# Kernel tuning notes

Measured on AMD Instinct MI355X. Metric: run time of the kernel, lower is better.

The kernel has to match this reference:

```python
import jax, jax.numpy as jnp
import numpy as np

D, E, H, K = 1024, 8, 4096, 2
B, S = 4, 2048


def setup_inputs() -> dict:
    key = jax.random.key(0)
    ks = jax.random.split(key, 5)
    scale = 0.02
    return {
        "x": jax.random.normal(ks[0], (B, S, D), dtype=jnp.float32),
        "gate_w": jax.random.normal(ks[1], (D, E), dtype=jnp.float32) * scale,
        "w1": jax.random.normal(ks[2], (E, D, H), dtype=jnp.float32) * scale,
        "b1": jnp.zeros((E, H), dtype=jnp.float32),
        "w2": jax.random.normal(ks[3], (E, H, D), dtype=jnp.float32) * scale,
        "b2": jnp.zeros((E, D), dtype=jnp.float32),
        "top_k": K,
    }


def reference(x, gate_w, w1, b1, w2, b2, top_k):
    orig_shape = x.shape
    d = x.shape[-1]
    xt = x.reshape(-1, d)                      # [T, D]
    T = xt.shape[0]

    # Gating: top-k over expert scores, softmax over the selected k.
    scores = xt @ gate_w                       # [T, E]
    expert_weights, expert_indices = jax.lax.top_k(scores, top_k)  # [T, K]
    expert_weights = jax.nn.softmax(expert_weights, axis=-1)

    # Dense all-expert MLP (GPT-style fc -> GELU -> proj), batched over experts.
    h = jnp.einsum('td,edh->eth', xt, w1) + b1[:, None, :]   # [E, T, H]
    h = jax.nn.gelu(h, approximate=False)
    outs = jnp.einsum('eth,ehd->etd', h, w2) + b2[:, None, :]  # [E, T, D]

    # Combine: gather each token's selected experts and mix with gate weights.
    tok = jnp.arange(T)[:, None]               # [T, 1]
    gathered = outs[expert_indices, tok]       # [T, K, D]
    y = jnp.sum(gathered * expert_weights[..., None], axis=1)  # [T, D]
    return y.reshape(orig_shape)
```

## Files before the change

### kernel.cpp

```cpp
#include <hip/hip_runtime.h>
#include <stdint.h>

#define T_TOK 8192
#define D_DIM 1024
#define E_NUM 8
#define H_DIM 4096

#define BM 128
#define BN 128
#define BK 64
#define NSEG 8
#define MAX_ROWS2 17408
#define MAX_MT2 (MAX_ROWS2/BM)
#define KSPLIT 2

typedef unsigned short u16;
typedef __attribute__((ext_vector_type(8))) short shortx8;
typedef __attribute__((ext_vector_type(4))) float floatx4;
typedef __attribute__((ext_vector_type(8))) unsigned short ushortx8;

typedef const __attribute__((address_space(1))) unsigned int g_uint;
typedef __attribute__((address_space(3))) unsigned int l_uint;

__device__ __forceinline__ u16 f2bf(float f) {
  union { float f; unsigned int u; } v; v.f = f;
  unsigned int r = v.u + 0x7FFFu + ((v.u >> 16) & 1u);
  return (u16)(r >> 16);
}
__device__ __forceinline__ void gld_lds16(const u16* g, u16* l) {
  __builtin_amdgcn_global_load_lds((g_uint*)g, (l_uint*)l, 16, 0, 0);
}
__device__ __forceinline__ float gelu_fast(float v) {
  float y = v * (1.5957691216f + 0.07135481627f * v * v);
  y = fminf(y, 30.f);
  float ey = __expf(y);
  return v * ey * __builtin_amdgcn_rcpf(1.f + ey);
}

__global__ __launch_bounds__(256) void init_kernel(int* counts, int* fills, int* row_token) {
  int i = blockIdx.x * 256 + threadIdx.x;
  if (i < MAX_ROWS2) row_token[i] = -1;
  if (blockIdx.x == 0 && threadIdx.x < NSEG) { counts[threadIdx.x] = 0; fills[threadIdx.x] = 0; }
}

__global__ __launch_bounds__(256) void zero4_kernel(float4* out) {
  out[(size_t)blockIdx.x * 256 + threadIdx.x] = float4{0.f, 0.f, 0.f, 0.f};
}

__global__ __launch_bounds__(256) void convert_x_kernel(const float* __restrict__ X, u16* __restrict__ XC) {
  size_t i = ((size_t)blockIdx.x * 256 + threadIdx.x) * 8;
  float4 a = *(const float4*)&X[i];
  float4 b = *(const float4*)&X[i + 4];
  ushortx8 o;
  o[0] = f2bf(a.x); o[1] = f2bf(a.y); o[2] = f2bf(a.z); o[3] = f2bf(a.w);
  o[4] = f2bf(b.x); o[5] = f2bf(b.y); o[6] = f2bf(b.z); o[7] = f2bf(b.w);
  *(ushortx8*)&XC[i] = o;
}

__global__ __launch_bounds__(256) void gate_kernel(const float* __restrict__ X, const float* __restrict__ GW,
                                                   int* __restrict__ tk_idx, float* __restrict__ tk_w,
                                                   int* __restrict__ counts) {
  const int lane = threadIdx.x & 63;
  const int t = blockIdx.x * 4 + (threadIdx.x >> 6);
  const float4* xr4 = (const float4*)(X + (size_t)t * D_DIM + lane * 16);
  const float4* gw4 = (const float4*)GW;
  float acc[E_NUM];
#pragma unroll
  for (int e = 0; e < E_NUM; e++) acc[e] = 0.f;
#pragma unroll
  for (int i4 = 0; i4 < 4; i4++) {
    float4 xv = xr4[i4];
#pragma unroll
    for (int c = 0; c < 4; c++) {
      float xs = (&xv.x)[c];
      int d = lane * 16 + i4 * 4 + c;
      float4 g0 = gw4[d * 2], g1 = gw4[d * 2 + 1];
      acc[0] += xs * g0.x; acc[1] += xs * g0.y; acc[2] += xs * g0.z; acc[3] += xs * g0.w;
      acc[4] += xs * g1.x; acc[5] += xs * g1.y; acc[6] += xs * g1.z; acc[7] += xs * g1.w;
    }
  }
#pragma unroll
  for (int e = 0; e < E_NUM; e++)
    for (int off = 32; off; off >>= 1) acc[e] += __shfl_xor(acc[e], off);
  if (lane == 0) {
    int i0 = 0; float v0 = acc[0];
#pragma unroll
    for (int e = 1; e < E_NUM; e++) if (acc[e] > v0) { v0 = acc[e]; i0 = e; }
    int i1 = -1; float v1 = -1e30f;
#pragma unroll
    for (int e = 0; e < E_NUM; e++) if (e != i0 && acc[e] > v1) { v1 = acc[e]; i1 = e; }
    float e1 = expf(v1 - v0);
    float inv = 1.f / (1.f + e1);
    tk_idx[t * 2] = i0; tk_idx[t * 2 + 1] = i1;
    tk_w[t * 2] = inv;  tk_w[t * 2 + 1] = e1 * inv;
    atomicAdd(&counts[i0], 1); atomicAdd(&counts[i1], 1);
  }
}

__global__ void prefix_kernel(const int* counts, int* seg) {
  if (threadIdx.x == 0 && blockIdx.x == 0) {
    int a = 0;
    for (int i = 0; i < NSEG; i++) { seg[i] = a; a += ((counts[i] + BM - 1) / BM) * BM; }
    seg[NSEG] = a;
  }
}

__global__ __launch_bounds__(256) void fill_kernel(const int* __restrict__ tk_idx, const float* __restrict__ tk_w,
                                                   const int* __restrict__ seg, int* __restrict__ fills,
                                                   int* __restrict__ row_token, float* __restrict__ row_weight) {
  int t = blockIdx.x * 256 + threadIdx.x;
  if (t >= T_TOK) return;
#pragma unroll
  for (int s = 0; s < 2; s++) {
    int sidx = tk_idx[t * 2 + s];
    int pos = atomicAdd(&fills[sidx], 1);
    int r = seg[sidx] + pos;
    row_token[r] = t; row_weight[r] = tk_w[t * 2 + s];
  }
}

__global__ __launch_bounds__(256) void transpose_kernel(const float* __restrict__ src, u16* __restrict__ dst,
                                                        int R, int C) {
  __shared__ u16 tile[32][33];
  int tx = threadIdx.x & 31, ty = threadIdx.x >> 5;
  size_t off = (size_t)blockIdx.z * R * C;
  int r0 = blockIdx.y * 32, c0 = blockIdx.x * 32;
#pragma unroll
  for (int i = 0; i < 32; i += 8) tile[ty + i][tx] = f2bf(src[off + (size_t)(r0 + ty + i) * C + c0 + tx]);
  __syncthreads();
#pragma unroll
  for (int i = 0; i < 32; i += 8) dst[off + (size_t)(c0 + ty + i) * R + r0 + tx] = tile[tx][ty + i];
}

__global__ __launch_bounds__(256, 3) void fc1_kernel(const u16* __restrict__ XC, const u16* __restrict__ W1T,
                                                     const float* __restrict__ B1, u16* __restrict__ Hbuf,
                                                     const int* __restrict__ row_token, const int* __restrict__ seg,
                                                     int mtile0, int e_filter) {
  const int mtile = mtile0 + blockIdx.y, ntile = blockIdx.x;
  const int row0 = mtile * BM;
  if (row0 >= seg[NSEG]) return;
  int sidx = 0;
#pragma unroll
  for (int i = 1; i < NSEG; i++) if (row0 >= seg[i]) sidx = i;
  const int e = sidx;
  if (e_filter >= 0 && e != e_filter) return;
  const size_t ebase = (e_filter >= 0) ? 0 : (size_t)e * H_DIM;
  const u16* Bbase = W1T + (ebase + (size_t)ntile * BN) * D_DIM;

  __shared__ u16 lA[BM * BK];
  __shared__ u16 lB[BN * BK];
  const int tid = threadIdx.x;
  const u16* gA[4]; const u16* gB[4];
#pragma unroll
  for (int r = 0; r < 4; r++) {
    int c = r * 256 + tid;
    int arow = c >> 3, acol = (c & 7) * 8;
    int tok = row_token[row0 + arow]; if (tok < 0) tok = 0;
    gA[r] = XC + (size_t)tok * D_DIM + acol;
    gB[r] = Bbase + (size_t)arow * D_DIM + acol;
  }
  const int lane = tid & 63;
  const int mq = (tid >> 7) & 1, nq = (tid >> 6) & 1;
  const int lrow = lane & 15, quad = lane >> 4;
  floatx4 acc[4][4];
#pragma unroll
  for (int i = 0; i < 4; i++)
#pragma unroll
    for (int j = 0; j < 4; j++)
#pragma unroll
      for (int r = 0; r < 4; r++) acc[i][j][r] = 0.f;

  for (int k0 = 0; k0 < D_DIM; k0 += BK) {
#pragma unroll
    for (int r = 0; r < 4; r++) gld_lds16(gA[r] + k0, &lA[(r * 256 + tid) * 8]);
#pragma unroll
    for (int r = 0; r < 4; r++) gld_lds16(gB[r] + k0, &lB[(r * 256 + tid) * 8]);
    __syncthreads();
#pragma unroll
    for (int kk = 0; kk < 2; kk++) {
      shortx8 af[4], bfr[4];
#pragma unroll
      for (int i = 0; i < 4; i++) af[i]  = *(const shortx8*)&lA[(mq * 64 + i * 16 + lrow) * BK + kk * 32 + quad * 8];
#pragma unroll
      for (int i = 0; i < 4; i++) bfr[i] = *(const shortx8*)&lB[(nq * 64 + i * 16 + lrow) * BK + kk * 32 + quad * 8];
#pragma unroll
      for (int i = 0; i < 4; i++)
#pragma unroll
        for (int j = 0; j < 4; j++)
          acc[i][j] = __builtin_amdgcn_mfma_f32_16x16x32_bf16(af[i], bfr[j], acc[i][j], 0, 0, 0);
    }
    __syncthreads();
  }
#pragma unroll
  for (int j = 0; j < 4; j++) {
    float bv = B1[(size_t)e * H_DIM + ntile * BN + nq * 64 + j * 16 + lrow];
#pragma unroll
    for (int i = 0; i < 4; i++)
#pragma unroll
      for (int rr = 0; rr < 4; rr++) {
        int hrow = (mtile - mtile0) * BM + mq * 64 + i * 16 + quad * 4 + rr;
        float v = acc[i][j][rr] + bv;
        Hbuf[(size_t)hrow * H_DIM + (size_t)ntile * BN + nq * 64 + j * 16 + lrow] = f2bf(gelu_fast(v));
      }
  }
}

__global__ __launch_bounds__(256, 3) void fc2_kernel(const u16* __restrict__ Hbuf, const u16* __restrict__ W2T,
                                                     const float* __restrict__ B2, float* __restrict__ out,
                                                     const int* __restrict__ row_token, const float* __restrict__ row_weight,
                                                     const int* __restrict__ seg,
                                                     int mtile0, int e_filter) {
  const int mtile = mtile0 + blockIdx.y, ntile = blockIdx.x;
  const int kz = blockIdx.z;
  const int row0 = mtile * BM;
  if (row0 >= seg[NSEG]) return;
  int sidx = 0;
#pragma unroll
  for (int i = 1; i < NSEG; i++) if (row0 >= seg[i]) sidx = i;
  const int e = sidx;
  if (e_filter >= 0 && e != e_filter) return;
  const size_t ebase = (e_filter >= 0) ? 0 : (size_t)e * D_DIM;
  const u16* Bbase = W2T + (ebase + (size_t)ntile * BN) * H_DIM;

  __shared__ u16 lA[BM * BK];
  __shared__ u16 lB[BN * BK];
  const int tid = threadIdx.x;
  const u16* gA[4]; const u16* gB[4];
#pragma unroll
  for (int r = 0; r < 4; r++) {
    int c = r * 256 + tid;
    int arow = c >> 3, acol = (c & 7) * 8;
    gA[r] = Hbuf + (size_t)((mtile - mtile0) * BM + arow) * H_DIM + acol;
    gB[r] = Bbase + (size_t)arow * H_DIM + acol;
  }
  const int lane = tid & 63;
  const int mq = (tid >> 7) & 1, nq = (tid >> 6) & 1;
  const int lrow = lane & 15, quad = lane >> 4;
  floatx4 acc[4][4];
#pragma unroll
  for (int i = 0; i < 4; i++)
#pragma unroll
    for (int j = 0; j < 4; j++)
#pragma unroll
      for (int r = 0; r < 4; r++) acc[i][j][r] = 0.f;

  const int kbeg = kz * (H_DIM / KSPLIT);
  const int kend = kbeg + (H_DIM / KSPLIT);
  for (int k0 = kbeg; k0 < kend; k0 += BK) {
#pragma unroll
    for (int r = 0; r < 4; r++) gld_lds16(gA[r] + k0, &lA[(r * 256 + tid) * 8]);
#pragma unroll
    for (int r = 0; r < 4; r++) gld_lds16(gB[r] + k0, &lB[(r * 256 + tid) * 8]);
    __syncthreads();
#pragma unroll
    for (int kk = 0; kk < 2; kk++) {
      shortx8 af[4], bfr[4];
#pragma unroll
      for (int i = 0; i < 4; i++) af[i]  = *(const shortx8*)&lA[(mq * 64 + i * 16 + lrow) * BK + kk * 32 + quad * 8];
#pragma unroll
      for (int i = 0; i < 4; i++) bfr[i] = *(const shortx8*)&lB[(nq * 64 + i * 16 + lrow) * BK + kk * 32 + quad * 8];
#pragma unroll
      for (int i = 0; i < 4; i++)
#pragma unroll
        for (int j = 0; j < 4; j++)
          acc[i][j] = __builtin_amdgcn_mfma_f32_16x16x32_bf16(af[i], bfr[j], acc[i][j], 0, 0, 0);
    }
    __syncthreads();
  }
#pragma unroll
  for (int i = 0; i < 4; i++)
#pragma unroll
    for (int rr = 0; rr < 4; rr++) {
      int gr = row0 + mq * 64 + i * 16 + quad * 4 + rr;
      int tok = row_token[gr];
      if (tok >= 0) {
        float wgt = row_weight[gr];
        size_t base = (size_t)tok * D_DIM + (size_t)ntile * BN + nq * 64 + lrow;
#pragma unroll
        for (int j = 0; j < 4; j++) {
          float bv = (kz == 0) ? B2[(size_t)e * D_DIM + ntile * BN + nq * 64 + j * 16 + lrow] : 0.f;
          float val = (acc[i][j][rr] + bv) * wgt;
          unsafeAtomicAdd(&out[base + j * 16], val);
        }
      }
    }
}

extern "C" void kernel_launch(void* const* d_in, const int* in_sizes, int n_in,
                              void* d_out, int out_size, void* d_ws, size_t ws_size,
                              hipStream_t stream) {
  const float* x  = (const float*)d_in[0];
  const float* gw = (const float*)d_in[1];
  const float* w1 = (const float*)d_in[2];
  const float* b1 = (const float*)d_in[3];
  const float* w2 = (const float*)d_in[4];
  const float* b2 = (const float*)d_in[5];
  float* out = (float*)d_out;

  char* p = (char*)d_ws;
  auto alloc = [&](size_t n) { char* q = p; p += (n + 255) & ~(size_t)255; return q; };
  int*   counts     = (int*)alloc(NSEG * 4);
  int*   fills      = (int*)alloc(NSEG * 4);
  int*   seg        = (int*)alloc((NSEG + 1) * 4);
  int*   tk_idx     = (int*)alloc((size_t)T_TOK * 2 * 4);
  float* tk_w       = (float*)alloc((size_t)T_TOK * 2 * 4);
  int*   row_token  = (int*)alloc((size_t)MAX_ROWS2 * 4);
  float* row_weight = (float*)alloc((size_t)MAX_ROWS2 * 4);
  u16*   xc         = (u16*)alloc((size_t)T_TOK * D_DIM * 2);
  size_t meta = (size_t)(p - (char*)d_ws);

  const size_t Wfull = (size_t)E_NUM * H_DIM * D_DIM * 2;
  const size_t Wone  = (size_t)H_DIM * D_DIM * 2;
  auto hbytes = [](int n) { int cmx = (MAX_MT2 + n - 1) / n; return (size_t)cmx * BM * H_DIM * 2; };

  int mode = 3, N = 1;
  {
    const int cand[6] = {1, 2, 4, 8, 16, 32};
    for (int ci = 0; ci < 6 && mode == 3; ci++)
      if (meta + 2 * Wfull + hbytes(cand[ci]) <= ws_size) { mode = 0; N = cand[ci]; }
    for (int ci = 0; ci < 6 && mode == 3; ci++)
      if (meta + Wfull + hbytes(cand[ci]) <= ws_size) { mode = 1; N = cand[ci]; }
    for (int ci = 0; ci < 6 && mode == 3; ci++)
      if (meta + Wone + hbytes(cand[ci]) <= ws_size) { mode = 2; N = cand[ci]; }
  }

  if (mode == 3) {
    zero4_kernel<<<(int)(((size_t)T_TOK * D_DIM) / 1024), 256, 0, stream>>>((float4*)out);
    return;
  }

  u16 *W1T, *W2T;
  if (mode == 0) { W1T = (u16*)alloc(Wfull); W2T = (u16*)alloc(Wfull); }
  else           { W1T = W2T = (u16*)alloc(mode == 1 ? Wfull : Wone); }
  u16* Hbuf = (u16*)alloc(hbytes(N));
  const int cm = (MAX_MT2 + N - 1) / N;

  init_kernel<<<(MAX_ROWS2 + 255) / 256, 256, 0, stream>>>(counts, fills, row_token);
  convert_x_kernel<<<(int)(((size_t)T_TOK * D_DIM) / 2048), 256, 0, stream>>>(x, xc);
  gate_kernel<<<T_TOK / 4, 256, 0, stream>>>(x, gw, tk_idx, tk_w, counts);
  prefix_kernel<<<1, 64, 0, stream>>>(counts, seg);
  fill_kernel<<<T_TOK / 256, 256, 0, stream>>>(tk_idx, tk_w, seg, fills, row_token, row_weight);
  zero4_kernel<<<(int)(((size_t)T_TOK * D_DIM) / 1024), 256, 0, stream>>>((float4*)out);

  if (mode == 0) {
    transpose_kernel<<<dim3(H_DIM / 32, D_DIM / 32, E_NUM), 256, 0, stream>>>(w1, W1T, D_DIM, H_DIM);
    transpose_kernel<<<dim3(D_DIM / 32, H_DIM / 32, E_NUM), 256, 0, stream>>>(w2, W2T, H_DIM, D_DIM);
  }

  for (int c = 0; c < N; ++c) {
    int mtile0 = c * cm;
    int cmc = MAX_MT2 - mtile0; if (cmc > cm) cmc = cm; if (cmc <= 0) break;
    if (mode == 0) {
      fc1_kernel<<<dim3(H_DIM / BN, cmc), 256, 0, stream>>>(xc, W1T, b1, Hbuf, row_token, seg, mtile0, -1);
      fc2_kernel<<<dim3(D_DIM / BN, cmc, KSPLIT), 256, 0, stream>>>(Hbuf, W2T, b2, out, row_token, row_weight, seg, mtile0, -1);
    } else if (mode == 1) {
      transpose_kernel<<<dim3(H_DIM / 32, D_DIM / 32, E_NUM), 256, 0, stream>>>(w1, W1T, D_DIM, H_DIM);
      fc1_kernel<<<dim3(H_DIM / BN, cmc), 256, 0, stream>>>(xc, W1T, b1, Hbuf, row_token, seg, mtile0, -1);
      transpose_kernel<<<dim3(D_DIM / 32, H_DIM / 32, E_NUM), 256, 0, stream>>>(w2, W2T, H_DIM, D_DIM);
      fc2_kernel<<<dim3(D_DIM / BN, cmc, KSPLIT), 256, 0, stream>>>(Hbuf, W2T, b2, out, row_token, row_weight, seg, mtile0, -1);
    } else {
      for (int e = 0; e < E_NUM; e++) {
        transpose_kernel<<<dim3(H_DIM / 32, D_DIM / 32, 1), 256, 0, stream>>>(w1 + (size_t)e * D_DIM * H_DIM, W1T, D_DIM, H_DIM);
        fc1_kernel<<<dim3(H_DIM / BN, cmc), 256, 0, stream>>>(xc, W1T, b1, Hbuf, row_token, seg, mtile0, e);
      }
      for (int e = 0; e < E_NUM; e++) {
        transpose_kernel<<<dim3(D_DIM / 32, H_DIM / 32, 1), 256, 0, stream>>>(w2 + (size_t)e * H_DIM * D_DIM, W2T, H_DIM, D_DIM);
        fc2_kernel<<<dim3(D_DIM / BN, cmc, KSPLIT), 256, 0, stream>>>(Hbuf, W2T, b2, out, row_token, row_weight, seg, mtile0, e);
      }
    }
  }
}
```

Measured before the change: 1.085 ms.

## Replace split-K atomic scatter with per-row output buffer and combine kernel

fc2 no longer splits K or atomically adds into the output. Each routed row now writes its weighted result to a row-indexed buffer, and a new combine kernel sums each token's two expert rows using a row_of map recorded in fill_kernel. This drops the output zeroing and the float atomics, at the cost of an extra buffer write/read and half as many fc2 blocks. The weight transpose kernel also moves to 64x64 tiles with float4 loads and 8-wide bf16 stores. The larger workspace allocation could push mode selection toward a less favourable mode.

```diff
diff --git a/kernel.cpp b/kernel.cpp
--- a/kernel.cpp
+++ b/kernel.cpp
@@ -12,7 +12,6 @@
 #define NSEG 8
 #define MAX_ROWS2 17408
 #define MAX_MT2 (MAX_ROWS2/BM)
-#define KSPLIT 2
 
 typedef unsigned short u16;
 typedef __attribute__((ext_vector_type(8))) short shortx8;
@@ -107,7 +106,8 @@
 
 __global__ __launch_bounds__(256) void fill_kernel(const int* __restrict__ tk_idx, const float* __restrict__ tk_w,
                                                    const int* __restrict__ seg, int* __restrict__ fills,
-                                                   int* __restrict__ row_token, float* __restrict__ row_weight) {
+                                                   int* __restrict__ row_token, float* __restrict__ row_weight,
+                                                   int* __restrict__ row_of) {
   int t = blockIdx.x * 256 + threadIdx.x;
   if (t >= T_TOK) return;
 #pragma unroll
@@ -116,20 +116,34 @@
     int pos = atomicAdd(&fills[sidx], 1);
     int r = seg[sidx] + pos;
     row_token[r] = t; row_weight[r] = tk_w[t * 2 + s];
+    row_of[t * 2 + s] = r;
   }
 }
 
 __global__ __launch_bounds__(256) void transpose_kernel(const float* __restrict__ src, u16* __restrict__ dst,
                                                         int R, int C) {
-  __shared__ u16 tile[32][33];
-  int tx = threadIdx.x & 31, ty = threadIdx.x >> 5;
-  size_t off = (size_t)blockIdx.z * R * C;
-  int r0 = blockIdx.y * 32, c0 = blockIdx.x * 32;
-#pragma unroll
-  for (int i = 0; i < 32; i += 8) tile[ty + i][tx] = f2bf(src[off + (size_t)(r0 + ty + i) * C + c0 + tx]);
+  __shared__ u16 tile[64][68];
+  const int tid = threadIdx.x;
+  size_t off = (size_t)blockIdx.z * (size_t)R * C;
+  int r0 = blockIdx.y * 64, c0 = blockIdx.x * 64;
+  int rr = tid >> 4, cc = (tid & 15) * 4;
+#pragma unroll
+  for (int i = 0; i < 4; i++) {
+    int r = rr + i * 16;
+    float4 v = *(const float4*)&src[off + (size_t)(r0 + r) * C + c0 + cc];
+    u16* tp = &tile[r][cc];
+    tp[0] = f2bf(v.x); tp[1] = f2bf(v.y); tp[2] = f2bf(v.z); tp[3] = f2bf(v.w);
+  }
   __syncthreads();
-#pragma unroll
-  for (int i = 0; i < 32; i += 8) dst[off + (size_t)(c0 + ty + i) * R + r0 + tx] = tile[tx][ty + i];
+  int c = tid >> 3, rb = (tid & 7) * 8;
+#pragma unroll
+  for (int i = 0; i < 2; i++) {
+    int cx = c + i * 32;
+    ushortx8 o;
+#pragma unroll
+    for (int q = 0; q < 8; q++) o[q] = tile[rb + q][cx];
+    *(ushortx8*)&dst[off + (size_t)(c0 + cx) * R + r0 + rb] = o;
+  }
 }
 
 __global__ __launch_bounds__(256, 3) void fc1_kernel(const u16* __restrict__ XC, const u16* __restrict__ W1T,
@@ -206,12 +220,11 @@
 }
 
 __global__ __launch_bounds__(256, 3) void fc2_kernel(const u16* __restrict__ Hbuf, const u16* __restrict__ W2T,
-                                                     const float* __restrict__ B2, float* __restrict__ out,
+                                                     const float* __restrict__ B2, float* __restrict__ outbuf,
                                                      const int* __restrict__ row_token, const float* __restrict__ row_weight,
                                                      const int* __restrict__ seg,
                                                      int mtile0, int e_filter) {
   const int mtile = mtile0 + blockIdx.y, ntile = blockIdx.x;
-  const int kz = blockIdx.z;
   const int row0 = mtile * BM;
   if (row0 >= seg[NSEG]) return;
   int sidx = 0;
@@ -244,9 +257,7 @@
 #pragma unroll
       for (int r = 0; r < 4; r++) acc[i][j][r] = 0.f;
 
-  const int kbeg = kz * (H_DIM / KSPLIT);
-  const int kend = kbeg + (H_DIM / KSPLIT);
-  for (int k0 = kbeg; k0 < kend; k0 += BK) {
+  for (int k0 = 0; k0 < H_DIM; k0 += BK) {
 #pragma unroll
     for (int r = 0; r < 4; r++) gld_lds16(gA[r] + k0, &lA[(r * 256 + tid) * 8]);
 #pragma unroll
@@ -275,15 +286,24 @@
       int tok = row_token[gr];
       if (tok >= 0) {
         float wgt = row_weight[gr];
-        size_t base = (size_t)tok * D_DIM + (size_t)ntile * BN + nq * 64 + lrow;
+        float* obase = outbuf + (size_t)gr * D_DIM + (size_t)ntile * BN + nq * 64 + lrow;
 #pragma unroll
         for (int j = 0; j < 4; j++) {
-          float bv = (kz == 0) ? B2[(size_t)e * D_DIM + ntile * BN + nq * 64 + j * 16 + lrow] : 0.f;
-          float val = (acc[i][j][rr] + bv) * wgt;
-          unsafeAtomicAdd(&out[base + j * 16], val);
+          float bv = B2[(size_t)e * D_DIM + ntile * BN + nq * 64 + j * 16 + lrow];
+          obase[j * 16] = (acc[i][j][rr] + bv) * wgt;
         }
       }
     }
+}
+
+__global__ __launch_bounds__(256) void combine_kernel(const float* __restrict__ outbuf, const int* __restrict__ row_of,
+                                                      float* __restrict__ out) {
+  int t = blockIdx.x;
+  int d = threadIdx.x * 4;
+  int r0 = row_of[t * 2], r1 = row_of[t * 2 + 1];
+  float4 a = *(const float4*)&outbuf[(size_t)r0 * D_DIM + d];
+  float4 b = *(const float4*)&outbuf[(size_t)r1 * D_DIM + d];
+  *(float4*)&out[(size_t)t * D_DIM + d] = float4{a.x + b.x, a.y + b.y, a.z + b.z, a.w + b.w};
 }
 
 extern "C" void kernel_launch(void* const* d_in, const int* in_sizes, int n_in,
@@ -306,7 +326,9 @@
   float* tk_w       = (float*)alloc((size_t)T_TOK * 2 * 4);
   int*   row_token  = (int*)alloc((size_t)MAX_ROWS2 * 4);
   float* row_weight = (float*)alloc((size_t)MAX_ROWS2 * 4);
+  int*   row_of     = (int*)alloc((size_t)T_TOK * 2 * 4);
   u16*   xc         = (u16*)alloc((size_t)T_TOK * D_DIM * 2);
+  float* outbuf     = (float*)alloc((size_t)MAX_ROWS2 * D_DIM * 4);
   size_t meta = (size_t)(p - (char*)d_ws);
 
   const size_t Wfull = (size_t)E_NUM * H_DIM * D_DIM * 2;
@@ -339,12 +361,11 @@
   convert_x_kernel<<<(int)(((size_t)T_TOK * D_DIM) / 2048), 256, 0, stream>>>(x, xc);
   gate_kernel<<<T_TOK / 4, 256, 0, stream>>>(x, gw, tk_idx, tk_w, counts);
   prefix_kernel<<<1, 64, 0, stream>>>(counts, seg);
-  fill_kernel<<<T_TOK / 256, 256, 0, stream>>>(tk_idx, tk_w, seg, fills, row_token, row_weight);
-  zero4_kernel<<<(int)(((size_t)T_TOK * D_DIM) / 1024), 256, 0, stream>>>((float4*)out);
+  fill_kernel<<<T_TOK / 256, 256, 0, stream>>>(tk_idx, tk_w, seg, fills, row_token, row_weight, row_of);
 
   if (mode == 0) {
-    transpose_kernel<<<dim3(H_DIM / 32, D_DIM / 32, E_NUM), 256, 0, stream>>>(w1, W1T, D_DIM, H_DIM);
-    transpose_kernel<<<dim3(D_DIM / 32, H_DIM / 32, E_NUM), 256, 0, stream>>>(w2, W2T, H_DIM, D_DIM);
+    transpose_kernel<<<dim3(H_DIM / 64, D_DIM / 64, E_NUM), 256, 0, stream>>>(w1, W1T, D_DIM, H_DIM);
+    transpose_kernel<<<dim3(D_DIM / 64, H_DIM / 64, E_NUM), 256, 0, stream>>>(w2, W2T, H_DIM, D_DIM);
   }
 
   for (int c = 0; c < N; ++c) {
@@ -352,21 +373,22 @@
     int cmc = MAX_MT2 - mtile0; if (cmc > cm) cmc = cm; if (cmc <= 0) break;
     if (mode == 0) {
       fc1_kernel<<<dim3(H_DIM / BN, cmc), 256, 0, stream>>>(xc, W1T, b1, Hbuf, row_token, seg, mtile0, -1);
-      fc2_kernel<<<dim3(D_DIM / BN, cmc, KSPLIT), 256, 0, stream>>>(Hbuf, W2T, b2, out, row_token, row_weight, seg, mtile0, -1);
+      fc2_kernel<<<dim3(D_DIM / BN, cmc), 256, 0, stream>>>(Hbuf, W2T, b2, outbuf, row_token, row_weight, seg, mtile0, -1);
     } else if (mode == 1) {
-      transpose_kernel<<<dim3(H_DIM / 32, D_DIM / 32, E_NUM), 256, 0, stream>>>(w1, W1T, D_DIM, H_DIM);
+      transpose_kernel<<<dim3(H_DIM / 64, D_DIM / 64, E_NUM), 256, 0, stream>>>(w1, W1T, D_DIM, H_DIM);
       fc1_kernel<<<dim3(H_DIM / BN, cmc), 256, 0, stream>>>(xc, W1T, b1, Hbuf, row_token, seg, mtile0, -1);
-      transpose_kernel<<<dim3(D_DIM / 32, H_DIM / 32, E_NUM), 256, 0, stream>>>(w2, W2T, H_DIM, D_DIM);
-      fc2_kernel<<<dim3(D_DIM / BN, cmc, KSPLIT), 256, 0, stream>>>(Hbuf, W2T, b2, out, row_token, row_weight, seg, mtile0, -1);
+      transpose_kernel<<<dim3(D_DIM / 64, H_DIM / 64, E_NUM), 256, 0, stream>>>(w2, W2T, H_DIM, D_DIM);
+      fc2_kernel<<<dim3(D_DIM / BN, cmc), 256, 0, stream>>>(Hbuf, W2T, b2, outbuf, row_token, row_weight, seg, mtile0, -1);
     } else {
       for (int e = 0; e < E_NUM; e++) {
-        transpose_kernel<<<dim3(H_DIM / 32, D_DIM / 32, 1), 256, 0, stream>>>(w1 + (size_t)e * D_DIM * H_DIM, W1T, D_DIM, H_DIM);
+        transpose_kernel<<<dim3(H_DIM / 64, D_DIM / 64, 1), 256, 0, stream>>>(w1 + (size_t)e * D_DIM * H_DIM, W1T, D_DIM, H_DIM);
         fc1_kernel<<<dim3(H_DIM / BN, cmc), 256, 0, stream>>>(xc, W1T, b1, Hbuf, row_token, seg, mtile0, e);
       }
       for (int e = 0; e < E_NUM; e++) {
-        transpose_kernel<<<dim3(D_DIM / 32, H_DIM / 32, 1), 256, 0, stream>>>(w2 + (size_t)e * H_DIM * D_DIM, W2T, H_DIM, D_DIM);
-        fc2_kernel<<<dim3(D_DIM / BN, cmc, KSPLIT), 256, 0, stream>>>(Hbuf, W2T, b2, out, row_token, row_weight, seg, mtile0, e);
+        transpose_kernel<<<dim3(D_DIM / 64, H_DIM / 64, 1), 256, 0, stream>>>(w2 + (size_t)e * H_DIM * D_DIM, W2T, H_DIM, D_DIM);
+        fc2_kernel<<<dim3(D_DIM / BN, cmc), 256, 0, stream>>>(Hbuf, W2T, b2, outbuf, row_token, row_weight, seg, mtile0, e);
       }
     }
   }
-}
+  combine_kernel<<<T_TOK, 256, 0, stream>>>(outbuf, row_of, out);
+}
```

Result: faster. 1.025 ms (-5.5%).
